# Kernel tuning notes

Measured on AMD Instinct MI355X. Metric: run time of the kernel, lower is better.

Reference implementation:

```python
import jax, jax.numpy as jnp
import numpy as np

DELTA_VAR = 0.5
DELTA_DIST = 1.5
ALPHA = 1.0
BETA = 1.0
GAMMA = 0.001
IGNORE = 0
C = 20  # static label count: max(target)+1 with labels drawn from [0, 20)


def setup_inputs() -> dict:
    key = jax.random.key(0)
    k1, k2 = jax.random.split(key)
    emb = jax.random.normal(k1, (4, 16, 400, 800), dtype=jnp.float32)
    target = jax.random.randint(k2, (4, 400, 800), 0, 20, dtype=jnp.int32)
    return {"emb": emb, "target": target}


def _safe_norm(sq):
    # L2 norm from squared distance with zero-safe sqrt (matches torch.norm fwd,
    # and gives finite grads at 0 like torch's subgradient convention)
    nz = sq > 0
    return jnp.sqrt(jnp.where(nz, sq, 1.0)) * nz.astype(sq.dtype)


def _loss_one(x, lab):
    # x: (E, H, W), lab: (H, W) int labels in [0, C)
    E = x.shape[0]
    xf = x.reshape(E, -1).T          # (P, E)
    lf = lab.reshape(-1)             # (P,)
    dt = xf.dtype

    counts = jax.ops.segment_sum(jnp.ones_like(lf, dtype=dt), lf, num_segments=C)  # (C,)
    sums = jax.ops.segment_sum(xf, lf, num_segments=C)                              # (C, E)
    means = sums / counts[:, None]                                                  # (C, E)

    keep = jnp.array([c for c in range(C) if c != IGNORE])  # static
    Ck = C - 1
    means_k = means[keep]            # (Ck, E)
    counts_k = counts[keep]          # (Ck,)

    # --- variance (pull) term: distance of each pixel to its own cluster mean ---
    mean_px = means[lf]                                   # (P, E) gather
    d = _safe_norm(jnp.sum((xf - mean_px) ** 2, axis=1))  # (P,)
    mask = (lf != IGNORE).astype(dt)
    hinge = mask * jnp.maximum(d - DELTA_VAR, 0.0) ** 2
    var_per_inst = jax.ops.segment_sum(hinge, lf, num_segments=C)[keep] / counts_k
    variance_term = jnp.sum(var_per_inst) / Ck

    # --- distance (push) term: pairwise hinge between kept cluster means ---
    diff = means_k[:, None, :] - means_k[None, :, :]      # (Ck, Ck, E)
    dm = _safe_norm(jnp.sum(diff ** 2, axis=-1))          # (Ck, Ck)
    repulsion = 2.0 * DELTA_DIST * (1.0 - jnp.eye(Ck, dtype=dt))
    hinged = jnp.maximum(repulsion - dm, 0.0) ** 2
    distance_term = jnp.sum(hinged) / (Ck * (Ck - 1))

    # --- regularizer: mean norm of cluster means ---
    reg_term = jnp.sum(_safe_norm(jnp.sum(means_k ** 2, axis=1))) / Ck

    return ALPHA * variance_term + BETA * distance_term + GAMMA * reg_term


def reference(emb, target):
    losses = jax.vmap(_loss_one)(emb, target)  # (N,)
    return (jnp.sum(losses) / emb.shape[0])[None]  # shape (1,) like torch
```

## Files before the change

### kernel.cpp

```cpp
#include <hip/hip_runtime.h>

#define N_IMG 4
#define E_DIM 16
#define G_PIX 80000
#define C_CLS 20
#define CK 19
#define NREP 8
#define EG 8
#define NEG (E_DIM / EG)
#define SL1 128
#define R1 (G_PIX / SL1)
#define GRID1 (SL1 * NEG * N_IMG)
#define SL2 256
#define R2 ((G_PIX + SL2 - 1) / SL2)
#define GRID2 (SL2 * N_IMG)
#define MSTRIDE 17
#define LS_SLOT 9
#define SCALE_F 16777216.0f
#define INV_SCALE (1.0f / 16777216.0f)

#define SUMS_OFF 0
#define CNT_OFF  (N_IMG * C_CLS * E_DIM * 8)
#define PART_OFF (CNT_OFF + N_IMG * C_CLS * 4)
#define WS_BYTES (PART_OFF + GRID2 * 4)

static_assert(G_PIX % SL1 == 0, "k_sums slicing must be exact");

__global__ __launch_bounds__(256, 4) void k_sums(const float* __restrict__ emb,
                                                 const int* __restrict__ target,
                                                 char* __restrict__ wsb) {
    __shared__ unsigned long long ls[C_CLS][NREP][LS_SLOT];
    __shared__ unsigned int lc[C_CLS][NREP];

    const int tid = threadIdx.x;
    const int b = blockIdx.x;
    const int n = b & 3;
    const int eg = (b >> 2) & (NEG - 1);
    const int slice = b >> 3;
    const int e0 = eg * EG;

    unsigned long long* lsf = &ls[0][0][0];
    for (int i = tid; i < C_CLS * NREP * LS_SLOT; i += 256) lsf[i] = 0ull;
    for (int i = tid; i < C_CLS * NREP; i += 256) (&lc[0][0])[i] = 0u;
    __syncthreads();

    const float4* emb0 = (const float4*)emb + ((size_t)(n * E_DIM + e0)) * G_PIX;
    const int4* tgt4 = (const int4*)target + (size_t)n * G_PIX;
    const int r = tid & (NREP - 1);

#define QADD(p, idx, val) \
    atomicAdd((p) + (idx), (unsigned long long)(long long)__float2int_rn((val) * SCALE_F))

    const int g1 = (slice + 1) * R1;
    for (int g = slice * R1 + tid; g < g1; g += 256) {
        const int4 lb = tgt4[g];
        float4 v[EG];
#pragma unroll
        for (int k = 0; k < EG; k++) v[k] = emb0[(size_t)k * G_PIX + g];

        unsigned long long* px = &ls[lb.x][r][0];
        unsigned long long* py = &ls[lb.y][r][0];
        unsigned long long* pz = &ls[lb.z][r][0];
        unsigned long long* pw = &ls[lb.w][r][0];
#pragma unroll
        for (int k = 0; k < EG; k++) {
            QADD(px, k, v[k].x);
            QADD(py, k, v[k].y);
            QADD(pz, k, v[k].z);
            QADD(pw, k, v[k].w);
        }
        if (eg == 0) {
            atomicAdd(&lc[lb.x][r], 1u); atomicAdd(&lc[lb.y][r], 1u);
            atomicAdd(&lc[lb.z][r], 1u); atomicAdd(&lc[lb.w][r], 1u);
        }
    }
#undef QADD
    __syncthreads();

    unsigned long long* gsum = (unsigned long long*)(wsb + SUMS_OFF);
    unsigned int* gcnt = (unsigned int*)(wsb + CNT_OFF);
    for (int i = tid; i < C_CLS * EG; i += 256) {
        const int c = i >> 3, e1 = i & 7;
        unsigned long long q = 0ull;
#pragma unroll
        for (int rr = 0; rr < NREP; rr++) q += ls[c][rr][e1];
        atomicAdd(&gsum[(n * C_CLS + c) * E_DIM + e0 + e1], q);
    }
    if (eg == 0) {
        for (int c = tid; c < C_CLS; c += 256) {
            unsigned int s = 0;
#pragma unroll
            for (int rr = 0; rr < NREP; rr++) s += lc[c][rr];
            atomicAdd(&gcnt[n * C_CLS + c], s);
        }
    }
}

__global__ __launch_bounds__(256, 4) void k_var(const float* __restrict__ emb,
                                                const int* __restrict__ target,
                                                char* __restrict__ wsb) {
    __shared__ float lmean[C_CLS * MSTRIDE];
    __shared__ float lw[C_CLS];
    __shared__ float red[256];

    const int tid = threadIdx.x;
    const int b = blockIdx.x;
    const int n = b & 3;
    const int s2 = b >> 2;

    const long long* gsum = (const long long*)(wsb + SUMS_OFF);
    const unsigned int* gcnt = (const unsigned int*)(wsb + CNT_OFF);

    for (int i = tid; i < C_CLS * E_DIM; i += 256) {
        const int c = i >> 4, e = i & 15;
        const float cnt = (float)gcnt[n * C_CLS + c];
        const float s = (float)gsum[n * C_CLS * E_DIM + i] * INV_SCALE;
        lmean[c * MSTRIDE + e] = (cnt > 0.f) ? s / cnt : 0.f;
    }
    if (tid < C_CLS) {
        const float cnt = (float)gcnt[n * C_CLS + tid];
        lw[tid] = (tid != 0 && cnt > 0.f) ? 1.0f / (cnt * (float)CK) : 0.f;
    }
    __syncthreads();

    float acc = 0.f;
    if (b < N_IMG) {
        for (int idx = tid; idx < CK * CK; idx += 256) {
            const int i = idx / CK + 1, j = idx % CK + 1;
            if (i != j) {
                float sq = 0.f;
#pragma unroll
                for (int e = 0; e < E_DIM; e++) {
                    const float d = lmean[i * MSTRIDE + e] - lmean[j * MSTRIDE + e];
                    sq += d * d;
                }
                const float dm = sqrtf(sq);
                const float h = fmaxf(3.0f - dm, 0.f);
                acc += h * h;
            }
        }
        acc *= 1.0f / (float)(CK * (CK - 1));
        float racc = 0.f;
        for (int c = tid + 1; c < C_CLS; c += 256) {
            float sq = 0.f;
#pragma unroll
            for (int e = 0; e < E_DIM; e++) {
                const float m = lmean[c * MSTRIDE + e];
                sq += m * m;
            }
            racc += sqrtf(sq);
        }
        acc += 0.001f * racc / (float)CK;
    }

    const float4* emb4 = (const float4*)emb + (size_t)n * E_DIM * G_PIX;
    const int4* tgt4 = (const int4*)target + (size_t)n * G_PIX;
    const int gend0 = (s2 + 1) * R2;
    const int gend = (gend0 < G_PIX) ? gend0 : G_PIX;
    for (int g = s2 * R2 + tid; g < gend; g += 256) {
        const int4 lb = tgt4[g];
        float4 v[E_DIM];
#pragma unroll
        for (int e = 0; e < E_DIM; e++) v[e] = emb4[(size_t)e * G_PIX + g];

        const int bx = lb.x * MSTRIDE, by = lb.y * MSTRIDE;
        const int bz = lb.z * MSTRIDE, bw = lb.w * MSTRIDE;
        float sx = 0.f, sy = 0.f, sz = 0.f, sw = 0.f;
#pragma unroll
        for (int e = 0; e < E_DIM; e++) {
            float d;
            d = v[e].x - lmean[bx + e]; sx += d * d;
            d = v[e].y - lmean[by + e]; sy += d * d;
            d = v[e].z - lmean[bz + e]; sz += d * d;
            d = v[e].w - lmean[bw + e]; sw += d * d;
        }
        float h;
        h = fmaxf(sqrtf(sx) - 0.5f, 0.f); acc += h * h * lw[lb.x];
        h = fmaxf(sqrtf(sy) - 0.5f, 0.f); acc += h * h * lw[lb.y];
        h = fmaxf(sqrtf(sz) - 0.5f, 0.f); acc += h * h * lw[lb.z];
        h = fmaxf(sqrtf(sw) - 0.5f, 0.f); acc += h * h * lw[lb.w];
    }

    red[tid] = acc;
    __syncthreads();
    for (int s = 128; s > 0; s >>= 1) {
        if (tid < s) red[tid] += red[tid + s];
        __syncthreads();
    }
    if (tid == 0) ((float*)(wsb + PART_OFF))[b] = red[0];
}

__global__ void k_fin(const char* __restrict__ wsb, float* __restrict__ out) {
    __shared__ float red[256];
    const int tid = threadIdx.x;
    const float* part = (const float*)(wsb + PART_OFF);
    float a = 0.f;
#pragma unroll
    for (int i = 0; i < GRID2 / 256; i++) a += part[i * 256 + tid];
    red[tid] = a;
    __syncthreads();
    for (int s = 128; s > 0; s >>= 1) {
        if (tid < s) red[tid] += red[tid + s];
        __syncthreads();
    }
    if (tid == 0) out[0] = red[0] * 0.25f;
}

extern "C" void kernel_launch(void* const* d_in, const int* in_sizes, int n_in,
                              void* d_out, int out_size, void* d_ws, size_t ws_size,
                              hipStream_t stream) {
    const float* emb = (const float*)d_in[0];
    const int* target = (const int*)d_in[1];
    float* out = (float*)d_out;
    char* wsb = (char*)d_ws;

    hipMemsetAsync(d_ws, 0, WS_BYTES, stream);
    k_sums<<<dim3(GRID1), 256, 0, stream>>>(emb, target, wsb);
    k_var<<<dim3(GRID2), 256, 0, stream>>>(emb, target, wsb);
    k_fin<<<1, 256, 0, stream>>>(wsb, out);
}
```

Measured before the change: 137.9 us.

## Merge embedding-group split in k_sums and fuse final reduction into k_var

k_sums now processes all 16 embedding dims per block instead of splitting them into two groups, halving the grid and avoiding duplicate label loads and block setup. The final partial-sum reduction kernel is folded into k_var using an agent-scope atomic done-counter so the last finishing block reduces the partials and writes the output. This removes one kernel launch, but raises LDS and register use per k_sums block and halves its block count, which may lower occupancy.

```diff
diff --git a/kernel.cpp b/kernel.cpp
--- a/kernel.cpp
+++ b/kernel.cpp
@@ -6,23 +6,22 @@
 #define C_CLS 20
 #define CK 19
 #define NREP 8
-#define EG 8
-#define NEG (E_DIM / EG)
 #define SL1 128
 #define R1 (G_PIX / SL1)
-#define GRID1 (SL1 * NEG * N_IMG)
+#define GRID1 (SL1 * N_IMG)
 #define SL2 256
 #define R2 ((G_PIX + SL2 - 1) / SL2)
 #define GRID2 (SL2 * N_IMG)
 #define MSTRIDE 17
-#define LS_SLOT 9
+#define LS_SLOT 17
 #define SCALE_F 16777216.0f
 #define INV_SCALE (1.0f / 16777216.0f)
 
 #define SUMS_OFF 0
 #define CNT_OFF  (N_IMG * C_CLS * E_DIM * 8)
 #define PART_OFF (CNT_OFF + N_IMG * C_CLS * 4)
-#define WS_BYTES (PART_OFF + GRID2 * 4)
+#define DONE_OFF (PART_OFF + GRID2 * 4)
+#define WS_BYTES (DONE_OFF + 4)
 
 static_assert(G_PIX % SL1 == 0, "k_sums slicing must be exact");
 
@@ -35,16 +34,14 @@
     const int tid = threadIdx.x;
     const int b = blockIdx.x;
     const int n = b & 3;
-    const int eg = (b >> 2) & (NEG - 1);
-    const int slice = b >> 3;
-    const int e0 = eg * EG;
+    const int slice = b >> 2;
 
     unsigned long long* lsf = &ls[0][0][0];
     for (int i = tid; i < C_CLS * NREP * LS_SLOT; i += 256) lsf[i] = 0ull;
     for (int i = tid; i < C_CLS * NREP; i += 256) (&lc[0][0])[i] = 0u;
     __syncthreads();
 
-    const float4* emb0 = (const float4*)emb + ((size_t)(n * E_DIM + e0)) * G_PIX;
+    const float4* emb0 = (const float4*)emb + (size_t)n * E_DIM * G_PIX;
     const int4* tgt4 = (const int4*)target + (size_t)n * G_PIX;
     const int r = tid & (NREP - 1);
 
@@ -54,54 +51,52 @@
     const int g1 = (slice + 1) * R1;
     for (int g = slice * R1 + tid; g < g1; g += 256) {
         const int4 lb = tgt4[g];
-        float4 v[EG];
-#pragma unroll
-        for (int k = 0; k < EG; k++) v[k] = emb0[(size_t)k * G_PIX + g];
+        float4 v[E_DIM];
+#pragma unroll
+        for (int k = 0; k < E_DIM; k++) v[k] = emb0[(size_t)k * G_PIX + g];
 
         unsigned long long* px = &ls[lb.x][r][0];
         unsigned long long* py = &ls[lb.y][r][0];
         unsigned long long* pz = &ls[lb.z][r][0];
         unsigned long long* pw = &ls[lb.w][r][0];
 #pragma unroll
-        for (int k = 0; k < EG; k++) {
+        for (int k = 0; k < E_DIM; k++) {
             QADD(px, k, v[k].x);
             QADD(py, k, v[k].y);
             QADD(pz, k, v[k].z);
             QADD(pw, k, v[k].w);
         }
-        if (eg == 0) {
-            atomicAdd(&lc[lb.x][r], 1u); atomicAdd(&lc[lb.y][r], 1u);
-            atomicAdd(&lc[lb.z][r], 1u); atomicAdd(&lc[lb.w][r], 1u);
-        }
+        atomicAdd(&lc[lb.x][r], 1u); atomicAdd(&lc[lb.y][r], 1u);
+        atomicAdd(&lc[lb.z][r], 1u); atomicAdd(&lc[lb.w][r], 1u);
     }
 #undef QADD
     __syncthreads();
 
     unsigned long long* gsum = (unsigned long long*)(wsb + SUMS_OFF);
     unsigned int* gcnt = (unsigned int*)(wsb + CNT_OFF);
-    for (int i = tid; i < C_CLS * EG; i += 256) {
-        const int c = i >> 3, e1 = i & 7;
+    for (int i = tid; i < C_CLS * E_DIM; i += 256) {
+        const int c = i >> 4, e = i & 15;
         unsigned long long q = 0ull;
 #pragma unroll
-        for (int rr = 0; rr < NREP; rr++) q += ls[c][rr][e1];
-        atomicAdd(&gsum[(n * C_CLS + c) * E_DIM + e0 + e1], q);
-    }
-    if (eg == 0) {
-        for (int c = tid; c < C_CLS; c += 256) {
-            unsigned int s = 0;
-#pragma unroll
-            for (int rr = 0; rr < NREP; rr++) s += lc[c][rr];
-            atomicAdd(&gcnt[n * C_CLS + c], s);
-        }
+        for (int rr = 0; rr < NREP; rr++) q += ls[c][rr][e];
+        atomicAdd(&gsum[(n * C_CLS + c) * E_DIM + e], q);
+    }
+    for (int c = tid; c < C_CLS; c += 256) {
+        unsigned int s = 0;
+#pragma unroll
+        for (int rr = 0; rr < NREP; rr++) s += lc[c][rr];
+        atomicAdd(&gcnt[n * C_CLS + c], s);
     }
 }
 
 __global__ __launch_bounds__(256, 4) void k_var(const float* __restrict__ emb,
                                                 const int* __restrict__ target,
-                                                char* __restrict__ wsb) {
+                                                char* __restrict__ wsb,
+                                                float* __restrict__ out) {
     __shared__ float lmean[C_CLS * MSTRIDE];
     __shared__ float lw[C_CLS];
     __shared__ float red[256];
+    __shared__ int last;
 
     const int tid = threadIdx.x;
     const int b = blockIdx.x;
@@ -187,23 +182,30 @@
         if (tid < s) red[tid] += red[tid + s];
         __syncthreads();
     }
-    if (tid == 0) ((float*)(wsb + PART_OFF))[b] = red[0];
-}
-
-__global__ void k_fin(const char* __restrict__ wsb, float* __restrict__ out) {
-    __shared__ float red[256];
-    const int tid = threadIdx.x;
-    const float* part = (const float*)(wsb + PART_OFF);
-    float a = 0.f;
-#pragma unroll
-    for (int i = 0; i < GRID2 / 256; i++) a += part[i * 256 + tid];
-    red[tid] = a;
-    __syncthreads();
-    for (int s = 128; s > 0; s >>= 1) {
-        if (tid < s) red[tid] += red[tid + s];
+
+    float* part = (float*)(wsb + PART_OFF);
+    unsigned* done = (unsigned*)(wsb + DONE_OFF);
+    if (tid == 0) {
+        part[b] = red[0];
+        __threadfence();
+        const unsigned arr = __hip_atomic_fetch_add(done, 1u, __ATOMIC_ACQ_REL,
+                                                    __HIP_MEMORY_SCOPE_AGENT);
+        last = (arr == GRID2 - 1) ? 1 : 0;
+    }
+    __syncthreads();
+
+    if (last) {
+        float a = 0.f;
+        for (int i = tid; i < GRID2; i += 256)
+            a += __hip_atomic_load(&part[i], __ATOMIC_RELAXED, __HIP_MEMORY_SCOPE_AGENT);
+        red[tid] = a;
         __syncthreads();
-    }
-    if (tid == 0) out[0] = red[0] * 0.25f;
+        for (int s = 128; s > 0; s >>= 1) {
+            if (tid < s) red[tid] += red[tid + s];
+            __syncthreads();
+        }
+        if (tid == 0) out[0] = red[0] * 0.25f;
+    }
 }
 
 extern "C" void kernel_launch(void* const* d_in, const int* in_sizes, int n_in,
@@ -216,6 +218,5 @@
 
     hipMemsetAsync(d_ws, 0, WS_BYTES, stream);
     k_sums<<<dim3(GRID1), 256, 0, stream>>>(emb, target, wsb);
-    k_var<<<dim3(GRID2), 256, 0, stream>>>(emb, target, wsb);
-    k_fin<<<1, 256, 0, stream>>>(wsb, out);
+    k_var<<<dim3(GRID2), 256, 0, stream>>>(emb, target, wsb, out);
 }
```

Measured after the change: 177.7 us. 28.8% more time.
